# Kernel optimization log

Hardware: AMD Instinct MI355X
Metric: run time of the kernel (lower is better)

## Reference

```python
import jax, jax.numpy as jnp
import numpy as np

N_FREQS = 6  # PositionEmbedding default used by LISA


def setup_inputs() -> dict:
    key = jax.random.key(0)
    ks = jax.random.split(key, 8)
    B, L, N, D, H = 8, 32768, 2048, 64, 256
    in_dim = 1 * (2 * N_FREQS + 1) + 3 * D  # 13 + 192 = 205

    def w(k, i, o):
        return jax.random.normal(k, (i, o), jnp.float32) * (1.0 / np.sqrt(i))

    return {
        "coord": jax.random.uniform(ks[0], (B, L, 1), jnp.float32),
        "latent": jax.random.normal(ks[1], (B, N, D), jnp.float32),
        "W0": w(ks[2], in_dim, H), "b0": jnp.zeros((H,), jnp.float32),
        "W1": w(ks[3], H, H), "b1": jnp.zeros((H,), jnp.float32),
        "W2": w(ks[4], H, H), "b2": jnp.zeros((H,), jnp.float32),
        "W3": w(ks[5], H, H), "b3": jnp.zeros((H,), jnp.float32),
        "W4": w(ks[6], H, 1), "b4": jnp.zeros((1,), jnp.float32),
    }


def reference(coord, latent, W0, b0, W1, b1, W2, b2, W3, b3, W4, b4):
    B, N, D = latent.shape
    # feat_unfold: concat shifted-prev / self / shifted-next along channels
    feat = jnp.swapaxes(latent, 1, 2)                                   # [B, D, N]
    feat_prev = jnp.concatenate([feat[:, :, :1], feat[:, :, :-1]], axis=2)
    feat_next = jnp.concatenate([feat[:, :, 1:], feat[:, :, -1:]], axis=2)
    feat = jnp.concatenate([feat_prev, feat, feat_next], axis=1)        # [B, 3D, N]

    # grid_sample(bilinear, padding_mode='border', align_corners=False) on a
    # 1-row image: y coordinate 0 hits row 0 exactly, so only x interpolates.
    # torch mapping: ix = ((gx + 1) * W - 1) / 2 with gx = coord*2 - 1
    ix = coord[..., 0] * N - 0.5                                        # [B, L]
    x0 = jnp.floor(ix)
    t = ix - x0                                                         # lerp weight
    i0 = jnp.clip(x0.astype(jnp.int32), 0, N - 1)                       # border clamp
    i1 = jnp.clip(x0.astype(jnp.int32) + 1, 0, N - 1)
    f0 = jnp.take_along_axis(feat, i0[:, None, :], axis=2)              # [B, 3D, L]
    f1 = jnp.take_along_axis(feat, i1[:, None, :], axis=2)
    sampled = (1.0 - t)[:, None, :] * f0 + t[:, None, :] * f1
    sampled = jnp.swapaxes(sampled, 1, 2)                               # [B, L, 3D]

    # positional encoding: [x, sin(f x), cos(f x) for f in 1,2,4,8,16,32]
    freqs = 2.0 ** jnp.arange(N_FREQS, dtype=jnp.float32)
    ang = coord * freqs                                                 # [B, L, 6]
    pe = jnp.stack([jnp.sin(ang), jnp.cos(ang)], axis=-1)
    pe = pe.reshape(ang.shape[0], ang.shape[1], 2 * N_FREQS)            # [B, L, 12]

    inp = jnp.concatenate([coord, pe, sampled], axis=-1)                # [B, L, 205]

    h = jax.nn.relu(inp @ W0 + b0)
    h = jax.nn.relu(h @ W1 + b1)
    h = jax.nn.relu(h @ W2 + b2)
    h = jax.nn.relu(h @ W3 + b3)
    return h @ W4 + b4                                                  # [B, L, 1]
```

## Files before the change

### kernel.cpp

```cpp
#include <hip/hip_runtime.h>
#include <hip/hip_bf16.h>

typedef unsigned short ushort_t;
typedef unsigned int uint_t;
typedef __attribute__((ext_vector_type(8))) short short8;
typedef __attribute__((ext_vector_type(4))) float float4v;
typedef __attribute__((ext_vector_type(4))) uint_t uint4v;

#define NLAT 2048
#define DLAT 64

#define PW_BASE 128
#define PW0_OFF 0
#define PW1_OFF 57344
#define PW2_OFF 122880
#define PW3_OFF 188416

__device__ __forceinline__ float b2f(ushort_t u) {
  union { uint_t i; float f; } v; v.i = ((uint_t)u) << 16; return v.f;
}
__device__ __forceinline__ ushort_t f2b(float f) {
  uint_t x = __float_as_uint(f);
  uint_t r = (x + 0x7fffu + ((x >> 16) & 1u)) >> 16;
  return (ushort_t)r;
}
__device__ __forceinline__ uint_t pack2(float lo, float hi) {
  float2 t; t.x = lo; t.y = hi;
  union { __hip_bfloat162 h; uint_t u; } cv;
  cv.h = __float22bfloat162_rn(t);
  return cv.u;
}
__device__ __forceinline__ int imin(int a, int b) { return a < b ? a : b; }
__device__ __forceinline__ int imax(int a, int b) { return a > b ? a : b; }

__device__ __forceinline__ float ldv(const float* p, long i)    { return p[i]; }
__device__ __forceinline__ float ldv(const ushort_t* p, long i) { return b2f(p[i]); }
__device__ __forceinline__ void stv(float* p, long i, float v)    { p[i] = v; }
__device__ __forceinline__ void stv(ushort_t* p, long i, float v) { p[i] = f2b(v); }

__device__ __forceinline__ float4 load4f(const float* p) { return *(const float4*)p; }
__device__ __forceinline__ float4 load4f(const ushort_t* p) {
  uint2 u = *(const uint2*)p;
  float4 r;
  r.x = b2f((ushort_t)(u.x & 0xffffu)); r.y = b2f((ushort_t)(u.x >> 16));
  r.z = b2f((ushort_t)(u.y & 0xffffu)); r.w = b2f((ushort_t)(u.y >> 16));
  return r;
}

__global__ void detect_mode(const ushort_t* __restrict__ lat, int* __restrict__ flag) {
  if (threadIdx.x == 0) *flag = 0;
  __syncthreads();
  int big = 0;
  for (int i = threadIdx.x; i < 1024; i += 64) {
    float v = b2f(lat[i]);
    if (!(fabsf(v) < 1e5f)) big = 1;
  }
  if (__any(big) && threadIdx.x == 0) *flag = 1;
}

template <typename TI>
__global__ void pack_w_t(const TI* __restrict__ W0, const TI* __restrict__ W1,
                         const TI* __restrict__ W2, const TI* __restrict__ W3,
                         ushort_t* __restrict__ pw, const int* __restrict__ flag, int want)
{
  if (*flag != want) return;
  int g = blockIdx.x * blockDim.x + threadIdx.x;
  if (g >= 31 * 1024) return;
  int lane = g & 63, q = lane >> 4;
  int mt   = (g >> 6) & 15;
  int ktg  = g >> 10;
  const TI* W; ushort_t* dst; int kt, KT; bool isw0 = false;
  if (ktg < 7)       { W = W0; dst = pw + PW0_OFF; kt = ktg;      KT = 7; isw0 = true; }
  else if (ktg < 15) { W = W1; dst = pw + PW1_OFF; kt = ktg - 7;  KT = 8; }
  else if (ktg < 23) { W = W2; dst = pw + PW2_OFF; kt = ktg - 15; KT = 8; }
  else               { W = W3; dst = pw + PW3_OFF; kt = ktg - 23; KT = 8; }
  int col = mt * 16 + (lane & 15);
  uint_t words[4];
#pragma unroll
  for (int h = 0; h < 4; ++h) {
    ushort_t vv[2];
#pragma unroll
    for (int e = 0; e < 2; ++e) {
      int j = 2 * h + e;
      int f = 32 * kt + 16 * (j >> 2) + 4 * q + (j & 3);
      int row = f;
      if (isw0) row = (f < 192) ? (13 + f) : (f == 192 ? 0 : (f <= 204 ? f - 192 : -1));
      vv[e] = (row >= 0) ? f2b(ldv(W, (long)row * 256 + col)) : (ushort_t)0;
    }
    words[h] = (uint_t)vv[0] | ((uint_t)vv[1] << 16);
  }
  uint4 o; o.x = words[0]; o.y = words[1]; o.z = words[2]; o.w = words[3];
  *(uint4*)(dst + ((size_t)(mt * KT + kt) * 64 + lane) * 8) = o;
}

template <int KT>
__device__ __forceinline__ void prefetch_A0(const ushort_t* __restrict__ pwl,
                                            short8 (&A0)[4], int lane, int wv)
{
  const ushort_t* abase = pwl + (((size_t)(4 * wv) * KT) * 64 + lane) * 8;
#pragma unroll
  for (int m = 0; m < 4; ++m)
    A0[m] = *(const short8*)(abase + (size_t)(m * KT) * 512);
}

template <int KT>
__device__ __forceinline__ void run_layer_new(const ushort_t* __restrict__ pwl,
                                              float4v (&acc)[4][4],
                                              const ushort_t* __restrict__ act,
                                              int lane, int wv, short8 (&A0)[4])
{
#pragma unroll
  for (int m = 0; m < 4; ++m)
#pragma unroll
    for (int p = 0; p < 4; ++p)
      acc[m][p] = (float4v){0.f, 0.f, 0.f, 0.f};

  const ushort_t* abase = pwl + (((size_t)(4 * wv) * KT) * 64 + lane) * 8;
  short8 A1[4];

#pragma unroll
  for (int kt = 0; kt < KT; ++kt) {
    short8 (&Ac)[4] = (kt & 1) ? A1 : A0;
    short8 (&An)[4] = (kt & 1) ? A0 : A1;
    if (kt + 1 < KT) {
#pragma unroll
      for (int m = 0; m < 4; ++m)
        An[m] = *(const short8*)(abase + (size_t)(m * KT + kt + 1) * 512);
    }
#pragma unroll
    for (int p = 0; p < 4; ++p) {
      short8 B = *(const short8*)&act[((size_t)(p * 8 + kt) * 64 + lane) * 8];
      acc[0][p] = __builtin_amdgcn_mfma_f32_16x16x32_bf16(Ac[0], B, acc[0][p], 0, 0, 0);
      acc[1][p] = __builtin_amdgcn_mfma_f32_16x16x32_bf16(Ac[1], B, acc[1][p], 0, 0, 0);
      acc[2][p] = __builtin_amdgcn_mfma_f32_16x16x32_bf16(Ac[2], B, acc[2][p], 0, 0, 0);
      acc[3][p] = __builtin_amdgcn_mfma_f32_16x16x32_bf16(Ac[3], B, acc[3][p], 0, 0, 0);
    }
  }
}

__device__ __forceinline__ void convert_store(float4v (&acc)[4][4],
                                              ushort_t* __restrict__ act,
                                              const float* __restrict__ bwl,
                                              int lane, int wv, int q)
{
  asm volatile("" ::: "memory");
  __builtin_amdgcn_s_barrier();
#pragma unroll
  for (int p2 = 0; p2 < 2; ++p2) {
    const float4 bE = *(const float4*)&bwl[wv * 64 + p2 * 32 + 4 * q];
    const float4 bO = *(const float4*)&bwl[wv * 64 + p2 * 32 + 16 + 4 * q];
    const int kt = 2 * wv + p2;
#pragma unroll
    for (int p = 0; p < 4; ++p) {
      const float4v& aE = acc[2 * p2][p];
      const float4v& aO = acc[2 * p2 + 1][p];
      uint4 o;
      o.x = pack2(fmaxf(aE[0] + bE.x, 0.f), fmaxf(aE[1] + bE.y, 0.f));
      o.y = pack2(fmaxf(aE[2] + bE.z, 0.f), fmaxf(aE[3] + bE.w, 0.f));
      o.z = pack2(fmaxf(aO[0] + bO.x, 0.f), fmaxf(aO[1] + bO.y, 0.f));
      o.w = pack2(fmaxf(aO[2] + bO.z, 0.f), fmaxf(aO[3] + bO.w, 0.f));
      *(uint4*)&act[((size_t)(p * 8 + kt) * 64 + lane) * 8] = o;
    }
  }
  asm volatile("s_waitcnt lgkmcnt(0)" ::: "memory");
  __builtin_amdgcn_s_barrier();
}

template <typename TI>
__global__ __launch_bounds__(256, 3) void lisa_fused_t(
    const TI* __restrict__ coord, const TI* __restrict__ latent,
    const TI* __restrict__ bias0, const TI* __restrict__ bias1,
    const TI* __restrict__ bias2, const TI* __restrict__ bias3,
    const TI* __restrict__ W4,    const TI* __restrict__ b4,
    const ushort_t* __restrict__ pw, TI* __restrict__ out,
    const int* __restrict__ flag, int want)
{
  if (*flag != want) return;
  __shared__ __align__(16) ushort_t act[4 * 8 * 64 * 8];
  __shared__ __align__(16) float bw[4 * 256 + 256 + 1];

  const int tid  = threadIdx.x;
  const int lane = tid & 63, q = lane >> 4, m15 = lane & 15;
  const int wv   = tid >> 6;
  const long pbase = (long)blockIdx.x * 64 + wv * 16 + m15;

  short8 A0[4];
  prefetch_A0<7>(pw + PW0_OFF, A0, lane, wv);

  for (int i = tid; i < 1281; i += 256) {
    float v;
    if (i < 256)       v = ldv(bias0, i);
    else if (i < 512)  v = ldv(bias1, i - 256);
    else if (i < 768)  v = ldv(bias2, i - 512);
    else if (i < 1024) v = ldv(bias3, i - 768);
    else if (i < 1280) v = ldv(W4, i - 1024);
    else               v = ldv(b4, 0);
    bw[i] = v;
  }

  {
    const long p = pbase;
    float c   = ldv(coord, p);
    float ixv = c * 2048.0f - 0.5f;
    float x0f = floorf(ixv);
    float t   = ixv - x0f;
    int   x0  = (int)x0f;
    int   i0  = imin(imax(x0, 0), NLAT - 1);
    int   i1  = imin(imax(x0 + 1, 0), NLAT - 1);
    float w0 = 1.0f - t, w1 = t;
    int rows0[3] = { imax(i0 - 1, 0), i0, imin(i0 + 1, NLAT - 1) };
    int rows1[3] = { imax(i1 - 1, 0), i1, imin(i1 + 1, NLAT - 1) };
    const TI* lat = latent + (size_t)(p >> 15) * (NLAT * DLAT);
    uint4v hu[7];
#pragma unroll
    for (int tb = 0; tb < 12; ++tb) {
      int region = tb >> 2;
      int d0 = 16 * (tb & 3) + 4 * q;
      float4 a = load4f(lat + (long)rows0[region] * DLAT + d0);
      float4 b = load4f(lat + (long)rows1[region] * DLAT + d0);
      hu[tb >> 1][(tb & 1) * 2 + 0] = pack2(w0 * a.x + w1 * b.x, w0 * a.y + w1 * b.y);
      hu[tb >> 1][(tb & 1) * 2 + 1] = pack2(w0 * a.z + w1 * b.z, w0 * a.w + w1 * b.w);
    }
    float pv[4];
#pragma unroll
    for (int s = 0; s < 4; ++s) {
      int f = 192 + 4 * q + s;
      float v = 0.0f;
      if (f == 192) v = c;
      else if (f <= 204) {
        int i = f - 193;
        float fr = (float)(1 << (i >> 1));
        float ang = c * fr;
        v = (i & 1) ? __cosf(ang) : __sinf(ang);
      }
      pv[s] = v;
    }
    hu[6][0] = pack2(pv[0], pv[1]);
    hu[6][1] = pack2(pv[2], pv[3]);
    hu[6][2] = 0; hu[6][3] = 0;

#pragma unroll
    for (int kt = 0; kt < 7; ++kt)
      *(uint4v*)&act[((size_t)(wv * 8 + kt) * 64 + lane) * 8] = hu[kt];
  }
  __syncthreads();

  float4v acc[4][4];

  run_layer_new<7>(pw + PW0_OFF, acc, act, lane, wv, A0);
  prefetch_A0<8>(pw + PW1_OFF, A0, lane, wv);
  convert_store(acc, act, bw + 0 * 256, lane, wv, q);
  run_layer_new<8>(pw + PW1_OFF, acc, act, lane, wv, A0);
  prefetch_A0<8>(pw + PW2_OFF, A0, lane, wv);
  convert_store(acc, act, bw + 1 * 256, lane, wv, q);
  run_layer_new<8>(pw + PW2_OFF, acc, act, lane, wv, A0);
  prefetch_A0<8>(pw + PW3_OFF, A0, lane, wv);
  convert_store(acc, act, bw + 2 * 256, lane, wv, q);
  run_layer_new<8>(pw + PW3_OFF, acc, act, lane, wv, A0);

  float psum[4] = {0.f, 0.f, 0.f, 0.f};
#pragma unroll
  for (int m = 0; m < 4; ++m) {
    const float4 b3v = *(const float4*)&bw[3 * 256 + wv * 64 + m * 16 + 4 * q];
    const float4 w4v = *(const float4*)&bw[1024 + wv * 64 + m * 16 + 4 * q];
#pragma unroll
    for (int p = 0; p < 4; ++p) {
      float v;
      v = fmaxf(acc[m][p][0] + b3v.x, 0.f); psum[p] += v * w4v.x;
      v = fmaxf(acc[m][p][1] + b3v.y, 0.f); psum[p] += v * w4v.y;
      v = fmaxf(acc[m][p][2] + b3v.z, 0.f); psum[p] += v * w4v.z;
      v = fmaxf(acc[m][p][3] + b3v.w, 0.f); psum[p] += v * w4v.w;
    }
  }
#pragma unroll
  for (int p = 0; p < 4; ++p) {
    psum[p] += __shfl_xor(psum[p], 16, 64);
    psum[p] += __shfl_xor(psum[p], 32, 64);
  }

  asm volatile("" ::: "memory");
  __builtin_amdgcn_s_barrier();
  float* part = (float*)act;
  if (lane < 16) {
#pragma unroll
    for (int p = 0; p < 4; ++p) part[wv * 64 + p * 16 + lane] = psum[p];
  }
  __syncthreads();
  if (tid < 64) {
    float s = part[tid] + part[64 + tid] + part[128 + tid] + part[192 + tid]
            + bw[1280];
    stv(out, (long)blockIdx.x * 64 + tid, s);
  }
}

extern "C" void kernel_launch(void* const* d_in, const int* in_sizes, int n_in,
                              void* d_out, int out_size, void* d_ws, size_t ws_size,
                              hipStream_t stream) {
  int* flag = (int*)d_ws;
  ushort_t* pw = (ushort_t*)d_ws + PW_BASE;

  detect_mode<<<1, 64, 0, stream>>>((const ushort_t*)d_in[1], flag);

  pack_w_t<float><<<62, 512, 0, stream>>>(
      (const float*)d_in[2], (const float*)d_in[4], (const float*)d_in[6],
      (const float*)d_in[8], pw, flag, 1);
  lisa_fused_t<float><<<4096, 256, 0, stream>>>(
      (const float*)d_in[0], (const float*)d_in[1],
      (const float*)d_in[3], (const float*)d_in[5], (const float*)d_in[7],
      (const float*)d_in[9], (const float*)d_in[10], (const float*)d_in[11],
      pw, (float*)d_out, flag, 1);

  pack_w_t<ushort_t><<<62, 512, 0, stream>>>(
      (const ushort_t*)d_in[2], (const ushort_t*)d_in[4], (const ushort_t*)d_in[6],
      (const ushort_t*)d_in[8], pw, flag, 0);
  lisa_fused_t<ushort_t><<<4096, 256, 0, stream>>>(
      (const ushort_t*)d_in[0], (const ushort_t*)d_in[1],
      (const ushort_t*)d_in[3], (const ushort_t*)d_in[5], (const ushort_t*)d_in[7],
      (const ushort_t*)d_in[9], (const ushort_t*)d_in[10], (const ushort_t*)d_in[11],
      pw, (ushort_t*)d_out, flag, 0);
}
```

Before: 227.6 us.

## Double-buffer LDS activations, prefetch B fragments, stagger wave access, raise MFMA priority

Splits the shared activation buffer into two ping-pong halves so each layer writes its output to the other buffer. This removes the barrier before convert_store and the one before the final partial-sum write. B operands are now software-prefetched from LDS one k-step ahead, alongside the existing A prefetch. Each wave starts at a rotated column block, (wv+i)&3, to spread LDS bank and port traffic, and MFMA blocks run under s_setprio(1). Doubling LDS to about 69 KB and holding more registers forces launch bounds to drop from 3 to 2 blocks per CU, so occupancy falls.

```diff
diff --git a/kernel.cpp b/kernel.cpp
--- a/kernel.cpp
+++ b/kernel.cpp
@@ -112,54 +112,67 @@
 #pragma unroll
   for (int m = 0; m < 4; ++m)
 #pragma unroll
-    for (int p = 0; p < 4; ++p)
-      acc[m][p] = (float4v){0.f, 0.f, 0.f, 0.f};
+    for (int i = 0; i < 4; ++i)
+      acc[m][i] = (float4v){0.f, 0.f, 0.f, 0.f};
 
   const ushort_t* abase = pwl + (((size_t)(4 * wv) * KT) * 64 + lane) * 8;
-  short8 A1[4];
+  short8 A1[4], B0[4], B1[4];
+
+  int boff[4];
+#pragma unroll
+  for (int i = 0; i < 4; ++i) boff[i] = (((wv + i) & 3) << 12) + (lane << 3);
+
+#pragma unroll
+  for (int i = 0; i < 4; ++i)
+    B0[i] = *(const short8*)&act[boff[i]];
 
 #pragma unroll
   for (int kt = 0; kt < KT; ++kt) {
     short8 (&Ac)[4] = (kt & 1) ? A1 : A0;
     short8 (&An)[4] = (kt & 1) ? A0 : A1;
+    short8 (&Bc)[4] = (kt & 1) ? B1 : B0;
+    short8 (&Bn)[4] = (kt & 1) ? B0 : B1;
     if (kt + 1 < KT) {
 #pragma unroll
       for (int m = 0; m < 4; ++m)
         An[m] = *(const short8*)(abase + (size_t)(m * KT + kt + 1) * 512);
-    }
-#pragma unroll
-    for (int p = 0; p < 4; ++p) {
-      short8 B = *(const short8*)&act[((size_t)(p * 8 + kt) * 64 + lane) * 8];
-      acc[0][p] = __builtin_amdgcn_mfma_f32_16x16x32_bf16(Ac[0], B, acc[0][p], 0, 0, 0);
-      acc[1][p] = __builtin_amdgcn_mfma_f32_16x16x32_bf16(Ac[1], B, acc[1][p], 0, 0, 0);
-      acc[2][p] = __builtin_amdgcn_mfma_f32_16x16x32_bf16(Ac[2], B, acc[2][p], 0, 0, 0);
-      acc[3][p] = __builtin_amdgcn_mfma_f32_16x16x32_bf16(Ac[3], B, acc[3][p], 0, 0, 0);
-    }
+#pragma unroll
+      for (int i = 0; i < 4; ++i)
+        Bn[i] = *(const short8*)&act[boff[i] + (kt + 1) * 512];
+    }
+    __builtin_amdgcn_s_setprio(1);
+#pragma unroll
+    for (int i = 0; i < 4; ++i) {
+      acc[0][i] = __builtin_amdgcn_mfma_f32_16x16x32_bf16(Ac[0], Bc[i], acc[0][i], 0, 0, 0);
+      acc[1][i] = __builtin_amdgcn_mfma_f32_16x16x32_bf16(Ac[1], Bc[i], acc[1][i], 0, 0, 0);
+      acc[2][i] = __builtin_amdgcn_mfma_f32_16x16x32_bf16(Ac[2], Bc[i], acc[2][i], 0, 0, 0);
+      acc[3][i] = __builtin_amdgcn_mfma_f32_16x16x32_bf16(Ac[3], Bc[i], acc[3][i], 0, 0, 0);
+    }
+    __builtin_amdgcn_s_setprio(0);
   }
 }
 
 __device__ __forceinline__ void convert_store(float4v (&acc)[4][4],
-                                              ushort_t* __restrict__ act,
+                                              ushort_t* __restrict__ actN,
                                               const float* __restrict__ bwl,
                                               int lane, int wv, int q)
 {
-  asm volatile("" ::: "memory");
-  __builtin_amdgcn_s_barrier();
 #pragma unroll
   for (int p2 = 0; p2 < 2; ++p2) {
     const float4 bE = *(const float4*)&bwl[wv * 64 + p2 * 32 + 4 * q];
     const float4 bO = *(const float4*)&bwl[wv * 64 + p2 * 32 + 16 + 4 * q];
     const int kt = 2 * wv + p2;
 #pragma unroll
-    for (int p = 0; p < 4; ++p) {
-      const float4v& aE = acc[2 * p2][p];
-      const float4v& aO = acc[2 * p2 + 1][p];
+    for (int i = 0; i < 4; ++i) {
+      const int p = (wv + i) & 3;
+      const float4v& aE = acc[2 * p2][i];
+      const float4v& aO = acc[2 * p2 + 1][i];
       uint4 o;
       o.x = pack2(fmaxf(aE[0] + bE.x, 0.f), fmaxf(aE[1] + bE.y, 0.f));
       o.y = pack2(fmaxf(aE[2] + bE.z, 0.f), fmaxf(aE[3] + bE.w, 0.f));
       o.z = pack2(fmaxf(aO[0] + bO.x, 0.f), fmaxf(aO[1] + bO.y, 0.f));
       o.w = pack2(fmaxf(aO[2] + bO.z, 0.f), fmaxf(aO[3] + bO.w, 0.f));
-      *(uint4*)&act[((size_t)(p * 8 + kt) * 64 + lane) * 8] = o;
+      *(uint4*)&actN[(size_t)(p << 12) + kt * 512 + (lane << 3)] = o;
     }
   }
   asm volatile("s_waitcnt lgkmcnt(0)" ::: "memory");
@@ -167,7 +180,7 @@
 }
 
 template <typename TI>
-__global__ __launch_bounds__(256, 3) void lisa_fused_t(
+__global__ __launch_bounds__(256, 2) void lisa_fused_t(
     const TI* __restrict__ coord, const TI* __restrict__ latent,
     const TI* __restrict__ bias0, const TI* __restrict__ bias1,
     const TI* __restrict__ bias2, const TI* __restrict__ bias3,
@@ -176,7 +189,7 @@
     const int* __restrict__ flag, int want)
 {
   if (*flag != want) return;
-  __shared__ __align__(16) ushort_t act[4 * 8 * 64 * 8];
+  __shared__ __align__(16) ushort_t act[2][4 * 8 * 64 * 8];
   __shared__ __align__(16) float bw[4 * 256 + 256 + 1];
 
   const int tid  = threadIdx.x;
@@ -241,22 +254,22 @@
 
 #pragma unroll
     for (int kt = 0; kt < 7; ++kt)
-      *(uint4v*)&act[((size_t)(wv * 8 + kt) * 64 + lane) * 8] = hu[kt];
+      *(uint4v*)&act[0][((size_t)(wv * 8 + kt) * 64 + lane) * 8] = hu[kt];
   }
   __syncthreads();
 
   float4v acc[4][4];
 
-  run_layer_new<7>(pw + PW0_OFF, acc, act, lane, wv, A0);
+  run_layer_new<7>(pw + PW0_OFF, acc, act[0], lane, wv, A0);
   prefetch_A0<8>(pw + PW1_OFF, A0, lane, wv);
-  convert_store(acc, act, bw + 0 * 256, lane, wv, q);
-  run_layer_new<8>(pw + PW1_OFF, acc, act, lane, wv, A0);
+  convert_store(acc, act[1], bw + 0 * 256, lane, wv, q);
+  run_layer_new<8>(pw + PW1_OFF, acc, act[1], lane, wv, A0);
   prefetch_A0<8>(pw + PW2_OFF, A0, lane, wv);
-  convert_store(acc, act, bw + 1 * 256, lane, wv, q);
-  run_layer_new<8>(pw + PW2_OFF, acc, act, lane, wv, A0);
+  convert_store(acc, act[0], bw + 1 * 256, lane, wv, q);
+  run_layer_new<8>(pw + PW2_OFF, acc, act[0], lane, wv, A0);
   prefetch_A0<8>(pw + PW3_OFF, A0, lane, wv);
-  convert_store(acc, act, bw + 2 * 256, lane, wv, q);
-  run_layer_new<8>(pw + PW3_OFF, acc, act, lane, wv, A0);
+  convert_store(acc, act[1], bw + 2 * 256, lane, wv, q);
+  run_layer_new<8>(pw + PW3_OFF, acc, act[1], lane, wv, A0);
 
   float psum[4] = {0.f, 0.f, 0.f, 0.f};
 #pragma unroll
@@ -264,26 +277,27 @@
     const float4 b3v = *(const float4*)&bw[3 * 256 + wv * 64 + m * 16 + 4 * q];
     const float4 w4v = *(const float4*)&bw[1024 + wv * 64 + m * 16 + 4 * q];
 #pragma unroll
-    for (int p = 0; p < 4; ++p) {
+    for (int i = 0; i < 4; ++i) {
       float v;
-      v = fmaxf(acc[m][p][0] + b3v.x, 0.f); psum[p] += v * w4v.x;
-      v = fmaxf(acc[m][p][1] + b3v.y, 0.f); psum[p] += v * w4v.y;
-      v = fmaxf(acc[m][p][2] + b3v.z, 0.f); psum[p] += v * w4v.z;
-      v = fmaxf(acc[m][p][3] + b3v.w, 0.f); psum[p] += v * w4v.w;
-    }
-  }
-#pragma unroll
-  for (int p = 0; p < 4; ++p) {
-    psum[p] += __shfl_xor(psum[p], 16, 64);
-    psum[p] += __shfl_xor(psum[p], 32, 64);
-  }
-
-  asm volatile("" ::: "memory");
-  __builtin_amdgcn_s_barrier();
-  float* part = (float*)act;
+      v = fmaxf(acc[m][i][0] + b3v.x, 0.f); psum[i] += v * w4v.x;
+      v = fmaxf(acc[m][i][1] + b3v.y, 0.f); psum[i] += v * w4v.y;
+      v = fmaxf(acc[m][i][2] + b3v.z, 0.f); psum[i] += v * w4v.z;
+      v = fmaxf(acc[m][i][3] + b3v.w, 0.f); psum[i] += v * w4v.w;
+    }
+  }
+#pragma unroll
+  for (int i = 0; i < 4; ++i) {
+    psum[i] += __shfl_xor(psum[i], 16, 64);
+    psum[i] += __shfl_xor(psum[i], 32, 64);
+  }
+
+  float* part = (float*)act[0];
   if (lane < 16) {
 #pragma unroll
-    for (int p = 0; p < 4; ++p) part[wv * 64 + p * 16 + lane] = psum[p];
+    for (int i = 0; i < 4; ++i) {
+      const int p = (wv + i) & 3;
+      part[wv * 64 + p * 16 + lane] = psum[i];
+    }
   }
   __syncthreads();
   if (tid < 64) {
```

Measured after the change: 229.5 us. No clear change (+0.8%).
